# Optimization experiments

Hardware: AMD Instinct MI355X
Metric: run time of the kernel (lower is better)

The kernel has to match this reference:

```python
import jax, jax.numpy as jnp
import numpy as np

LR = 1.0
THRESHOLD = 0.5
EPS = 1e-8


def _hebbian_mask(x, H):
    # x: [B, x_size], H: [y_size, x_size]
    xn = x / jnp.linalg.norm(x, axis=1, keepdims=True)
    y = xn @ H.T                                   # [B, y_size]
    yn = y / jnp.linalg.norm(y, axis=1, keepdims=True)
    theta = jnp.mean(yn ** 2)                      # scalar
    # sum over batch of outer products == GEMM: [y_size, x_size]
    H_new = H + LR * (jnp.einsum('by,bx->yx', yn, xn) - theta * H)
    score = jnp.sum(H_new, axis=1)                 # [y_size]
    score = (score - jnp.min(score)) / (jnp.max(score) - jnp.min(score) + EPS)
    return jnp.where(score < THRESHOLD, 0.0, 1.0).astype(x.dtype)


def setup_inputs() -> dict:
    key = jax.random.key(0)
    ks = jax.random.split(key, 12)
    B, D_IN, D_OUT = 8192, 1024, 1000
    h = [256, 128, 64]
    inp = {
        'x': jax.random.normal(ks[0], (B, D_IN), dtype=jnp.float32),
        'mask0': jnp.ones((h[0],), dtype=jnp.float32),
        'mask1': jnp.ones((h[1],), dtype=jnp.float32),
        'mask2': jnp.ones((h[2],), dtype=jnp.float32),
        # linear layer params (torch Linear: y = x @ W.T + b)
        'W1': jax.random.normal(ks[1], (h[0], D_IN), dtype=jnp.float32) * 0.02,
        'b1': jnp.zeros((h[0],), dtype=jnp.float32),
        'W2': jax.random.normal(ks[2], (h[1], h[0]), dtype=jnp.float32) * 0.02,
        'b2': jnp.zeros((h[1],), dtype=jnp.float32),
        'W3': jax.random.normal(ks[3], (h[2], h[1]), dtype=jnp.float32) * 0.02,
        'b3': jnp.zeros((h[2],), dtype=jnp.float32),
        'W4': jax.random.normal(ks[4], (D_OUT, h[2]), dtype=jnp.float32) * 0.02,
        'b4': jnp.zeros((D_OUT,), dtype=jnp.float32),
        # hebbian params, init N(0, 0.01) as in the module (4th never used in forward)
        'H1': jax.random.normal(ks[5], (h[0], D_IN), dtype=jnp.float32) * 0.01,
        'H2': jax.random.normal(ks[6], (h[1], h[0]), dtype=jnp.float32) * 0.01,
        'H3': jax.random.normal(ks[7], (h[2], h[1]), dtype=jnp.float32) * 0.01,
    }
    return inp


def reference(x, mask0, mask1, mask2, W1, b1, W2, b2, W3, b3, W4, b4, H1, H2, H3):
    # layer 1 (hebbian uses the layer *input*)
    hm0 = _hebbian_mask(x, H1)
    x1 = jax.nn.relu(x @ W1.T + b1) * mask0
    # layer 2
    hm1 = _hebbian_mask(x1, H2)
    x2 = jax.nn.relu(x1 @ W2.T + b2) * mask1
    # layer 3
    hm2 = _hebbian_mask(x2, H3)
    x3 = jax.nn.relu(x2 @ W3.T + b3) * mask2
    # layer 4 (relu applied, no mask, no hebbian)
    out = jax.nn.relu(x3 @ W4.T + b4)
    return (out, hm0, hm1, hm2)
```

## Files before the change

kernel.cpp:

```cpp
#include <hip/hip_runtime.h>
#include <math.h>

typedef __attribute__((ext_vector_type(8))) short short8;
typedef __attribute__((ext_vector_type(4))) float floatx4;

typedef __attribute__((address_space(1))) const unsigned int as1_uint;
typedef __attribute__((address_space(3))) unsigned int as3_uint;
#define GLD16(g, l) __builtin_amdgcn_global_load_lds((as1_uint*)(g), (as3_uint*)(l), 16, 0, 0)

__device__ __forceinline__ unsigned short f2bf(float f) {
    unsigned int u = __float_as_uint(f);
    return (unsigned short)((u + 0x7fffu + ((u >> 16) & 1u)) >> 16);
}
__device__ __forceinline__ float bf2f(unsigned short h) {
    return __uint_as_float(((unsigned int)h) << 16);
}

__global__ __launch_bounds__(256) void convert_x(
    const float* __restrict__ x, unsigned short* __restrict__ Axhl,
    float* __restrict__ rs1, float* __restrict__ rq1,
    float* __restrict__ rs2, float* __restrict__ rq2,
    float* __restrict__ rs3, float* __restrict__ rq3,
    float* __restrict__ score, int* __restrict__ ctr)
{
    const int row = blockIdx.x, tid = threadIdx.x;
    if (row == 0) { score[tid] = 0.f; if (tid < 8) ctr[tid] = 0; }
    if (tid == 0) { rs2[row] = 0.f; rq2[row] = 0.f; rs3[row] = 0.f; rq3[row] = 0.f; }
    float4 v = *(const float4*)(x + (size_t)row * 1024 + (tid << 2));
    ushort4 h, l;
    h.x = f2bf(v.x); l.x = f2bf(v.x - bf2f(h.x));
    h.y = f2bf(v.y); l.y = f2bf(v.y - bf2f(h.y));
    h.z = f2bf(v.z); l.z = f2bf(v.z - bf2f(h.z));
    h.w = f2bf(v.w); l.w = f2bf(v.w - bf2f(h.w));
    *(ushort4*)(Axhl + (size_t)row * 2048 + (tid << 2)) = h;
    *(ushort4*)(Axhl + (size_t)row * 2048 + 1024 + (tid << 2)) = l;
    float s = v.x + v.y + v.z + v.w;
    float qq = v.x*v.x + v.y*v.y + v.z*v.z + v.w*v.w;
#pragma unroll
    for (int d = 1; d < 64; d <<= 1) { s += __shfl_xor(s, d, 64); qq += __shfl_xor(qq, d, 64); }
    __shared__ float sS[4], sQ[4];
    if ((tid & 63) == 0) { sS[tid >> 6] = s; sQ[tid >> 6] = qq; }
    __syncthreads();
    if (tid == 0) {
        rs1[row] = sS[0] + sS[1] + sS[2] + sS[3];
        rq1[row] = sQ[0] + sQ[1] + sQ[2] + sQ[3];
    }
}

__global__ __launch_bounds__(256) void convert_w(
    const float* __restrict__ H1, const float* __restrict__ W1,
    const float* __restrict__ H2, const float* __restrict__ W2,
    const float* __restrict__ H3, const float* __restrict__ W3,
    const float* __restrict__ W4,
    unsigned short* __restrict__ B1, unsigned short* __restrict__ B2,
    unsigned short* __restrict__ B3, unsigned short* __restrict__ B4,
    float* __restrict__ rsH1, float* __restrict__ rsH2, float* __restrict__ rsH3)
{
    const int b = blockIdx.x, tid = threadIdx.x;
    const float* src; unsigned short* dst; int K; float* rsum = nullptr;
    if (b < 256)      { K = 1024; src = H1 + (size_t)b * 1024;        dst = B1 + (size_t)b * 2048;        rsum = rsH1 + b; }
    else if (b < 512) { K = 1024; src = W1 + (size_t)(b - 256) * 1024; dst = B1 + (size_t)b * 2048; }
    else if (b < 640) { K = 256;  src = H2 + (size_t)(b - 512) * 256;  dst = B2 + (size_t)(b - 512) * 512; rsum = rsH2 + (b - 512); }
    else if (b < 768) { K = 256;  src = W2 + (size_t)(b - 640) * 256;  dst = B2 + (size_t)(b - 512) * 512; }
    else if (b < 832) { K = 128;  src = H3 + (size_t)(b - 768) * 128;  dst = B3 + (size_t)(b - 768) * 256; rsum = rsH3 + (b - 768); }
    else if (b < 896) { K = 128;  src = W3 + (size_t)(b - 832) * 128;  dst = B3 + (size_t)(b - 768) * 256; }
    else { K = 64; int r = b - 896; src = (r < 1000) ? (W4 + (size_t)r * 64) : nullptr; dst = B4 + (size_t)r * 128; }

    float lsum = 0.f;
    if (tid * 4 < K) {
        float4 v = src ? *(const float4*)(src + tid * 4) : make_float4(0.f, 0.f, 0.f, 0.f);
        ushort4 h, l;
        h.x = f2bf(v.x); l.x = f2bf(v.x - bf2f(h.x));
        h.y = f2bf(v.y); l.y = f2bf(v.y - bf2f(h.y));
        h.z = f2bf(v.z); l.z = f2bf(v.z - bf2f(h.z));
        h.w = f2bf(v.w); l.w = f2bf(v.w - bf2f(h.w));
        *(ushort4*)(dst + tid * 4) = h;
        *(ushort4*)(dst + K + tid * 4) = l;
        lsum = v.x + v.y + v.z + v.w;
    }
    if (rsum) {
#pragma unroll
        for (int d = 1; d < 64; d <<= 1) lsum += __shfl_xor(lsum, d, 64);
        __shared__ float sS[4];
        if ((tid & 63) == 0) sS[tid >> 6] = lsum;
        __syncthreads();
        if (tid == 0) *rsum = sS[0] + sS[1] + sS[2] + sS[3];
    }
}

template<int TM, int TN>
__global__ __launch_bounds__(256) void mfma_layer(
    const unsigned short* __restrict__ Ag, const unsigned short* __restrict__ Bg,
    const float* __restrict__ bias, const float* __restrict__ maskv,
    float* __restrict__ T, unsigned short* __restrict__ Xhl,
    float* __restrict__ outF,
    float* __restrict__ rs, float* __restrict__ rq,
    int K, int Nh, int Nw, int NwReal)
{
    constexpr int MI = TM / 32;
    constexpr int NJ = TN / 32;
    constexpr int IA = TM / 16;
    constexpr int IB = TN / 16;
    constexpr int NI = 2 * (IA + IB);
    constexpr int PERW = NI / 4;
    constexpr int BUFB = NI * 1024;
    __shared__ __align__(16) char lds[2 * BUFB];

    const int tid = threadIdx.x;
    const int w = tid >> 6, lane = tid & 63;
    const int q = lane >> 4, m16 = lane & 15;
    const int wm = w & 1, wn = w >> 1;

    const int lin = blockIdx.y * gridDim.x + blockIdx.x;
    const int g = lin & 7, idx = lin >> 3;
    const int rows8 = gridDim.y >> 3;
    const int by = g + 8 * (idx % rows8);
    const int bx = idx / rows8;

    const int strideB = 4 * K;
    const int v = lane >> 2, u = lane & 3;

    const char* srcp[PERW];
#pragma unroll
    for (int t0 = 0; t0 < PERW; ++t0) {
        const int t = w * PERW + t0;
        int rloc; const char* base;
        if (t < IA)               { rloc = t * 16 + v;                base = (const char*)Ag + (size_t)(by * TM + rloc) * strideB; }
        else if (t < 2 * IA)      { rloc = (t - IA) * 16 + v;         base = (const char*)Ag + (size_t)(by * TM + rloc) * strideB + 2 * K; }
        else if (t < 2 * IA + IB) { rloc = (t - 2 * IA) * 16 + v;     base = (const char*)Bg + (size_t)(bx * TN + rloc) * strideB; }
        else                      { rloc = (t - 2 * IA - IB) * 16 + v; base = (const char*)Bg + (size_t)(bx * TN + rloc) * strideB + 2 * K; }
        srcp[t0] = base + ((u ^ (rloc & 3)) << 4);
    }

    auto stage = [&](int buf, int k0) {
        char* dst = lds + buf * BUFB + (w * PERW) * 1024;
        const int kb = 2 * k0;
#pragma unroll
        for (int t0 = 0; t0 < PERW; ++t0)
            GLD16(srcp[t0] + kb, dst + t0 * 1024);
    };

    floatx4 acc[MI][NJ] = {};
    const int NIT = K / 32;

    stage(0, 0);
    int cur = 0;
    for (int it = 0; it < NIT; ++it) {
        __syncthreads();
        if (it + 1 < NIT) stage(cur ^ 1, (it + 1) * 32);
        const char* pb = lds + cur * BUFB;
        short8 ah[MI], al[MI], bh[NJ], bl[NJ];
#pragma unroll
        for (int i = 0; i < MI; ++i) {
            const int ra = wm * (TM / 2) + i * 16 + m16;
            const int so = (q ^ (ra & 3)) << 4;
            ah[i] = *(const short8*)(pb + ra * 64 + so);
            al[i] = *(const short8*)(pb + IA * 1024 + ra * 64 + so);
        }
#pragma unroll
        for (int j = 0; j < NJ; ++j) {
            const int rb = wn * (TN / 2) + j * 16 + m16;
            const int so = (q ^ (rb & 3)) << 4;
            bh[j] = *(const short8*)(pb + 2 * IA * 1024 + rb * 64 + so);
            bl[j] = *(const short8*)(pb + (2 * IA + IB) * 1024 + rb * 64 + so);
        }
#pragma unroll
        for (int i = 0; i < MI; ++i)
#pragma unroll
            for (int j = 0; j < NJ; ++j) {
                acc[i][j] = __builtin_amdgcn_mfma_f32_16x16x32_bf16(ah[i], bh[j], acc[i][j], 0, 0, 0);
                acc[i][j] = __builtin_amdgcn_mfma_f32_16x16x32_bf16(al[i], bh[j], acc[i][j], 0, 0, 0);
                acc[i][j] = __builtin_amdgcn_mfma_f32_16x16x32_bf16(ah[i], bl[j], acc[i][j], 0, 0, 0);
            }
        cur ^= 1;
    }

    const int colW = bx * TN + wn * (TN / 2);
    const bool isHwave = (outF == nullptr) && (colW < Nh);
#pragma unroll
    for (int i = 0; i < MI; ++i) {
        const int row0 = by * TM + wm * (TM / 2) + i * 16 + q * 4;
        float rsum[4] = {0.f, 0.f, 0.f, 0.f}, rqsum[4] = {0.f, 0.f, 0.f, 0.f};
#pragma unroll
        for (int j = 0; j < NJ; ++j) {
            const int col = colW + j * 16 + m16;
            floatx4 vv = acc[i][j];
            if (outF) {
                if (col < NwReal) {
                    const float bb = bias[col];
#pragma unroll
                    for (int rg = 0; rg < 4; ++rg)
                        outF[(size_t)(row0 + rg) * NwReal + col] = fmaxf(vv[rg] + bb, 0.f);
                }
            } else if (isHwave) {
#pragma unroll
                for (int rg = 0; rg < 4; ++rg)
                    T[(size_t)(row0 + rg) * Nh + col] = vv[rg];
            } else {
                const int c = col - Nh;
                const float bb = bias[c], mm = maskv[c];
#pragma unroll
                for (int rg = 0; rg < 4; ++rg) {
                    const float xv = fmaxf(vv[rg] + bb, 0.f) * mm;
                    const unsigned short hi = f2bf(xv);
                    const unsigned short lo = f2bf(xv - bf2f(hi));
                    Xhl[(size_t)(row0 + rg) * (2 * Nw) + c] = hi;
                    Xhl[(size_t)(row0 + rg) * (2 * Nw) + Nw + c] = lo;
                    rsum[rg] += xv; rqsum[rg] += xv * xv;
                }
            }
        }
        if (rs && !isHwave && !outF) {
#pragma unroll
            for (int rg = 0; rg < 4; ++rg) {
                float a_ = rsum[rg], b_ = rqsum[rg];
#pragma unroll
                for (int d = 1; d < 16; d <<= 1) {
                    a_ += __shfl_xor(a_, d, 64);
                    b_ += __shfl_xor(b_, d, 64);
                }
                if (m16 == 0) {
                    atomicAdd(&rs[row0 + rg], a_);
                    atomicAdd(&rq[row0 + rg], b_);
                }
            }
        }
    }
}

__global__ __launch_bounds__(256) void hebb_finish(
    const float* __restrict__ T, const float* __restrict__ rs,
    const float* __restrict__ rq, const float* __restrict__ rowsumH,
    float* __restrict__ score, int* __restrict__ counter,
    float* __restrict__ hm, int ysize)
{
    const int tid = threadIdx.x, lane = tid & 63, wave = tid >> 6;
    const int vecsz = ysize >> 6;
    const int b0 = blockIdx.x * 64;
    float accv[4] = {0.f, 0.f, 0.f, 0.f};
    for (int r = wave; r < 64; r += 4) {
        const float* Trow = T + (size_t)(b0 + r) * ysize;
        float vals[4] = {0.f, 0.f, 0.f, 0.f};
        if (vecsz == 4) { float4 t = *(const float4*)(Trow + (lane << 2)); vals[0]=t.x; vals[1]=t.y; vals[2]=t.z; vals[3]=t.w; }
        else if (vecsz == 2) { float2 t = *(const float2*)(Trow + (lane << 1)); vals[0]=t.x; vals[1]=t.y; }
        else vals[0] = Trow[lane];
        float sq = vals[0]*vals[0] + vals[1]*vals[1] + vals[2]*vals[2] + vals[3]*vals[3];
#pragma unroll
        for (int i = 1; i < 64; i <<= 1) sq += __shfl_xor(sq, i, 64);
        const float wgt = rs[b0 + r] / (sqrtf(rq[b0 + r]) * sqrtf(sq));
        for (int j = 0; j < 4; ++j) accv[j] += vals[j] * wgt;
    }
    __shared__ float sPart[4][256];
    for (int j = 0; j < vecsz; ++j) sPart[wave][lane * vecsz + j] = accv[j];
    __syncthreads();
    if (tid < ysize)
        atomicAdd(&score[tid], sPart[0][tid] + sPart[1][tid] + sPart[2][tid] + sPart[3][tid]);
    __syncthreads();
    __shared__ int lastFlag;
    if (tid == 0) {
        __threadfence();
        lastFlag = (atomicAdd(counter, 1) == (int)gridDim.x - 1) ? 1 : 0;
    }
    __syncthreads();
    if (!lastFlag) return;
    float full = 0.f;
    if (tid < ysize) {
        float sc = atomicAdd(&score[tid], 0.f);
        full = (1.f - 1.f / (float)ysize) * rowsumH[tid] + sc;
    }
    __shared__ float sMin[256], sMax[256];
    sMin[tid] = (tid < ysize) ? full : 3.4e38f;
    sMax[tid] = (tid < ysize) ? full : -3.4e38f;
    __syncthreads();
    for (int st = 128; st > 0; st >>= 1) {
        if (tid < st) { sMin[tid] = fminf(sMin[tid], sMin[tid+st]); sMax[tid] = fmaxf(sMax[tid], sMax[tid+st]); }
        __syncthreads();
    }
    if (tid < ysize) {
        float nrm = (full - sMin[0]) / (sMax[0] - sMin[0] + 1e-8f);
        hm[tid] = (nrm < 0.5f) ? 0.f : 1.f;
    }
    score[tid] = 0.f;
}

extern "C" void kernel_launch(void* const* d_in, const int* in_sizes, int n_in,
                              void* d_out, int out_size, void* d_ws, size_t ws_size,
                              hipStream_t stream)
{
    const float* x     = (const float*)d_in[0];
    const float* mask0 = (const float*)d_in[1];
    const float* mask1 = (const float*)d_in[2];
    const float* mask2 = (const float*)d_in[3];
    const float* W1 = (const float*)d_in[4];  const float* b1 = (const float*)d_in[5];
    const float* W2 = (const float*)d_in[6];  const float* b2 = (const float*)d_in[7];
    const float* W3 = (const float*)d_in[8];  const float* b3 = (const float*)d_in[9];
    const float* W4 = (const float*)d_in[10]; const float* b4 = (const float*)d_in[11];
    const float* H1 = (const float*)d_in[12];
    const float* H2 = (const float*)d_in[13];
    const float* H3 = (const float*)d_in[14];

    float* out = (float*)d_out;
    float* hm0 = out + (size_t)8192 * 1000;
    float* hm1 = hm0 + 256;
    float* hm2 = hm1 + 128;

    float* ws = (float*)d_ws;
    unsigned short* Axhl = (unsigned short*)ws;
    unsigned short* X2hl = (unsigned short*)ws;
    unsigned short* X3hl = (unsigned short*)(ws + 1048576);
    float* p = ws + 8388608;
    unsigned short* B1 = (unsigned short*)p;  p += 524288;
    unsigned short* B2 = (unsigned short*)p;  p += 65536;
    unsigned short* B3 = (unsigned short*)p;  p += 16384;
    unsigned short* B4 = (unsigned short*)p;  p += 65536;
    float* T    = p;  p += 2097152;
    unsigned short* X1hl = (unsigned short*)p; p += 2097152;
    float* rs1 = p; p += 8192;  float* rq1 = p; p += 8192;
    float* rs2 = p; p += 8192;  float* rq2 = p; p += 8192;
    float* rs3 = p; p += 8192;  float* rq3 = p; p += 8192;
    float* rsH1 = p; p += 256;  float* rsH2 = p; p += 128;  float* rsH3 = p; p += 64;
    float* score = p; p += 256;
    int* ctr = (int*)p;

    convert_x<<<8192, 256, 0, stream>>>(x, Axhl, rs1, rq1, rs2, rq2, rs3, rq3, score, ctr);
    convert_w<<<1920, 256, 0, stream>>>(H1, W1, H2, W2, H3, W3, W4, B1, B2, B3, B4, rsH1, rsH2, rsH3);

    mfma_layer<128, 64><<<dim3(8, 64), 256, 0, stream>>>(
        Axhl, B1, b1, mask0, T, X1hl, nullptr, rs2, rq2, 1024, 256, 256, 256);
    hebb_finish<<<128, 256, 0, stream>>>(T, rs1, rq1, rsH1, score, ctr + 0, hm0, 256);

    mfma_layer<64, 64><<<dim3(4, 128), 256, 0, stream>>>(
        X1hl, B2, b2, mask1, T, X2hl, nullptr, rs3, rq3, 256, 128, 128, 128);
    hebb_finish<<<128, 256, 0, stream>>>(T, rs2, rq2, rsH2, score, ctr + 1, hm1, 128);

    mfma_layer<64, 64><<<dim3(2, 128), 256, 0, stream>>>(
        X2hl, B3, b3, mask2, T, X3hl, nullptr, nullptr, nullptr, 128, 64, 64, 64);
    hebb_finish<<<128, 256, 0, stream>>>(T, rs3, rq3, rsH3, score, ctr + 2, hm2, 64);

    mfma_layer<128, 64><<<dim3(16, 64), 256, 0, stream>>>(
        X3hl, B4, b4, nullptr, nullptr, nullptr, out, nullptr, nullptr, 64, 0, 1024, 1000);
}
```

Baseline: 225.8 us.

## Merge conversion kernels and fold hebbian reductions into next layer's GEMM launch

Combines the x and weight conversion kernels into one launch. Each hebb_finish reduction now runs as extra leading blocks inside the following layer's GEMM kernel, which needs separate T buffers and score arrays per layer. This cuts the launch count from 9 to 5 and lets the hebbian reduction run alongside the GEMM blocks. The LDS swizzle also changes to XOR with (row>>1)&3, aiming to reduce bank conflicts. The cost is more workspace and hebbian blocks that compete with GEMM blocks for compute units.

```diff
diff --git a/kernel.cpp b/kernel.cpp
--- a/kernel.cpp
+++ b/kernel.cpp
@@ -16,86 +16,147 @@
     return __uint_as_float(((unsigned int)h) << 16);
 }
 
-__global__ __launch_bounds__(256) void convert_x(
+__global__ __launch_bounds__(256) void convert_all(
     const float* __restrict__ x, unsigned short* __restrict__ Axhl,
-    float* __restrict__ rs1, float* __restrict__ rq1,
-    float* __restrict__ rs2, float* __restrict__ rq2,
-    float* __restrict__ rs3, float* __restrict__ rq3,
-    float* __restrict__ score, int* __restrict__ ctr)
-{
-    const int row = blockIdx.x, tid = threadIdx.x;
-    if (row == 0) { score[tid] = 0.f; if (tid < 8) ctr[tid] = 0; }
-    if (tid == 0) { rs2[row] = 0.f; rq2[row] = 0.f; rs3[row] = 0.f; rq3[row] = 0.f; }
-    float4 v = *(const float4*)(x + (size_t)row * 1024 + (tid << 2));
-    ushort4 h, l;
-    h.x = f2bf(v.x); l.x = f2bf(v.x - bf2f(h.x));
-    h.y = f2bf(v.y); l.y = f2bf(v.y - bf2f(h.y));
-    h.z = f2bf(v.z); l.z = f2bf(v.z - bf2f(h.z));
-    h.w = f2bf(v.w); l.w = f2bf(v.w - bf2f(h.w));
-    *(ushort4*)(Axhl + (size_t)row * 2048 + (tid << 2)) = h;
-    *(ushort4*)(Axhl + (size_t)row * 2048 + 1024 + (tid << 2)) = l;
-    float s = v.x + v.y + v.z + v.w;
-    float qq = v.x*v.x + v.y*v.y + v.z*v.z + v.w*v.w;
-#pragma unroll
-    for (int d = 1; d < 64; d <<= 1) { s += __shfl_xor(s, d, 64); qq += __shfl_xor(qq, d, 64); }
-    __shared__ float sS[4], sQ[4];
-    if ((tid & 63) == 0) { sS[tid >> 6] = s; sQ[tid >> 6] = qq; }
-    __syncthreads();
-    if (tid == 0) {
-        rs1[row] = sS[0] + sS[1] + sS[2] + sS[3];
-        rq1[row] = sQ[0] + sQ[1] + sQ[2] + sQ[3];
-    }
-}
-
-__global__ __launch_bounds__(256) void convert_w(
     const float* __restrict__ H1, const float* __restrict__ W1,
     const float* __restrict__ H2, const float* __restrict__ W2,
     const float* __restrict__ H3, const float* __restrict__ W3,
     const float* __restrict__ W4,
     unsigned short* __restrict__ B1, unsigned short* __restrict__ B2,
     unsigned short* __restrict__ B3, unsigned short* __restrict__ B4,
-    float* __restrict__ rsH1, float* __restrict__ rsH2, float* __restrict__ rsH3)
+    float* __restrict__ rs1, float* __restrict__ rq1,
+    float* __restrict__ rs2, float* __restrict__ rq2,
+    float* __restrict__ rs3, float* __restrict__ rq3,
+    float* __restrict__ rsH1, float* __restrict__ rsH2, float* __restrict__ rsH3,
+    float* __restrict__ score1, float* __restrict__ score2,
+    float* __restrict__ score3, int* __restrict__ ctr)
 {
     const int b = blockIdx.x, tid = threadIdx.x;
-    const float* src; unsigned short* dst; int K; float* rsum = nullptr;
-    if (b < 256)      { K = 1024; src = H1 + (size_t)b * 1024;        dst = B1 + (size_t)b * 2048;        rsum = rsH1 + b; }
-    else if (b < 512) { K = 1024; src = W1 + (size_t)(b - 256) * 1024; dst = B1 + (size_t)b * 2048; }
-    else if (b < 640) { K = 256;  src = H2 + (size_t)(b - 512) * 256;  dst = B2 + (size_t)(b - 512) * 512; rsum = rsH2 + (b - 512); }
-    else if (b < 768) { K = 256;  src = W2 + (size_t)(b - 640) * 256;  dst = B2 + (size_t)(b - 512) * 512; }
-    else if (b < 832) { K = 128;  src = H3 + (size_t)(b - 768) * 128;  dst = B3 + (size_t)(b - 768) * 256; rsum = rsH3 + (b - 768); }
-    else if (b < 896) { K = 128;  src = W3 + (size_t)(b - 832) * 128;  dst = B3 + (size_t)(b - 768) * 256; }
-    else { K = 64; int r = b - 896; src = (r < 1000) ? (W4 + (size_t)r * 64) : nullptr; dst = B4 + (size_t)r * 128; }
-
-    float lsum = 0.f;
-    if (tid * 4 < K) {
-        float4 v = src ? *(const float4*)(src + tid * 4) : make_float4(0.f, 0.f, 0.f, 0.f);
+    if (b < 8192) {
+        if (b == 0) {
+            score1[tid] = 0.f; score2[tid] = 0.f; score3[tid] = 0.f;
+            if (tid < 8) ctr[tid] = 0;
+        }
+        if (tid == 0) { rs2[b] = 0.f; rq2[b] = 0.f; rs3[b] = 0.f; rq3[b] = 0.f; }
+        float4 v = *(const float4*)(x + (size_t)b * 1024 + (tid << 2));
         ushort4 h, l;
         h.x = f2bf(v.x); l.x = f2bf(v.x - bf2f(h.x));
         h.y = f2bf(v.y); l.y = f2bf(v.y - bf2f(h.y));
         h.z = f2bf(v.z); l.z = f2bf(v.z - bf2f(h.z));
         h.w = f2bf(v.w); l.w = f2bf(v.w - bf2f(h.w));
-        *(ushort4*)(dst + tid * 4) = h;
-        *(ushort4*)(dst + K + tid * 4) = l;
-        lsum = v.x + v.y + v.z + v.w;
-    }
-    if (rsum) {
-#pragma unroll
-        for (int d = 1; d < 64; d <<= 1) lsum += __shfl_xor(lsum, d, 64);
-        __shared__ float sS[4];
-        if ((tid & 63) == 0) sS[tid >> 6] = lsum;
+        *(ushort4*)(Axhl + (size_t)b * 2048 + (tid << 2)) = h;
+        *(ushort4*)(Axhl + (size_t)b * 2048 + 1024 + (tid << 2)) = l;
+        float s = v.x + v.y + v.z + v.w;
+        float qq = v.x*v.x + v.y*v.y + v.z*v.z + v.w*v.w;
+#pragma unroll
+        for (int d = 1; d < 64; d <<= 1) { s += __shfl_xor(s, d, 64); qq += __shfl_xor(qq, d, 64); }
+        __shared__ float sS[4], sQ[4];
+        if ((tid & 63) == 0) { sS[tid >> 6] = s; sQ[tid >> 6] = qq; }
         __syncthreads();
-        if (tid == 0) *rsum = sS[0] + sS[1] + sS[2] + sS[3];
+        if (tid == 0) {
+            rs1[b] = sS[0] + sS[1] + sS[2] + sS[3];
+            rq1[b] = sQ[0] + sQ[1] + sQ[2] + sQ[3];
+        }
+    } else {
+        const int wb = b - 8192;
+        const float* src; unsigned short* dst; int K; float* rsum = nullptr;
+        if (wb < 256)      { K = 1024; src = H1 + (size_t)wb * 1024;         dst = B1 + (size_t)wb * 2048;        rsum = rsH1 + wb; }
+        else if (wb < 512) { K = 1024; src = W1 + (size_t)(wb - 256) * 1024; dst = B1 + (size_t)wb * 2048; }
+        else if (wb < 640) { K = 256;  src = H2 + (size_t)(wb - 512) * 256;  dst = B2 + (size_t)(wb - 512) * 512; rsum = rsH2 + (wb - 512); }
+        else if (wb < 768) { K = 256;  src = W2 + (size_t)(wb - 640) * 256;  dst = B2 + (size_t)(wb - 512) * 512; }
+        else if (wb < 832) { K = 128;  src = H3 + (size_t)(wb - 768) * 128;  dst = B3 + (size_t)(wb - 768) * 256; rsum = rsH3 + (wb - 768); }
+        else if (wb < 896) { K = 128;  src = W3 + (size_t)(wb - 832) * 128;  dst = B3 + (size_t)(wb - 768) * 256; }
+        else { K = 64; int r = wb - 896; src = (r < 1000) ? (W4 + (size_t)r * 64) : nullptr; dst = B4 + (size_t)r * 128; }
+        float lsum = 0.f;
+        if (tid * 4 < K) {
+            float4 v = src ? *(const float4*)(src + tid * 4) : make_float4(0.f, 0.f, 0.f, 0.f);
+            ushort4 h, l;
+            h.x = f2bf(v.x); l.x = f2bf(v.x - bf2f(h.x));
+            h.y = f2bf(v.y); l.y = f2bf(v.y - bf2f(h.y));
+            h.z = f2bf(v.z); l.z = f2bf(v.z - bf2f(h.z));
+            h.w = f2bf(v.w); l.w = f2bf(v.w - bf2f(h.w));
+            *(ushort4*)(dst + tid * 4) = h;
+            *(ushort4*)(dst + K + tid * 4) = l;
+            lsum = v.x + v.y + v.z + v.w;
+        }
+        if (rsum) {
+#pragma unroll
+            for (int d = 1; d < 64; d <<= 1) lsum += __shfl_xor(lsum, d, 64);
+            __shared__ float sW[4];
+            if ((tid & 63) == 0) sW[tid >> 6] = lsum;
+            __syncthreads();
+            if (tid == 0) *rsum = sW[0] + sW[1] + sW[2] + sW[3];
+        }
+    }
+}
+
+__device__ void hebb_dev(char* smem, int hb,
+    const float* __restrict__ T, const float* __restrict__ rs,
+    const float* __restrict__ rq, const float* __restrict__ rowsumH,
+    float* __restrict__ score, int* __restrict__ counter,
+    float* __restrict__ hm, int ysize, int nHebb)
+{
+    float* sPart = (float*)smem;
+    float* sMin  = sPart + 1024;
+    float* sMax  = sMin + 256;
+    int*   lastFlag = (int*)(sMax + 256);
+    const int tid = threadIdx.x, lane = tid & 63, wave = tid >> 6;
+    const int vecsz = ysize >> 6;
+    const int b0 = hb * 64;
+    float accv[4] = {0.f, 0.f, 0.f, 0.f};
+    for (int r = wave; r < 64; r += 4) {
+        const float* Trow = T + (size_t)(b0 + r) * ysize;
+        float vals[4] = {0.f, 0.f, 0.f, 0.f};
+        if (vecsz == 4)      { float4 t = *(const float4*)(Trow + (lane << 2)); vals[0]=t.x; vals[1]=t.y; vals[2]=t.z; vals[3]=t.w; }
+        else if (vecsz == 2) { float2 t = *(const float2*)(Trow + (lane << 1)); vals[0]=t.x; vals[1]=t.y; }
+        else                 vals[0] = Trow[lane];
+        float sq = vals[0]*vals[0] + vals[1]*vals[1] + vals[2]*vals[2] + vals[3]*vals[3];
+#pragma unroll
+        for (int i = 1; i < 64; i <<= 1) sq += __shfl_xor(sq, i, 64);
+        const float wgt = rs[b0 + r] / (sqrtf(rq[b0 + r]) * sqrtf(sq));
+        for (int j = 0; j < 4; ++j) accv[j] += vals[j] * wgt;
+    }
+    for (int j = 0; j < vecsz; ++j) sPart[wave * 256 + lane * vecsz + j] = accv[j];
+    __syncthreads();
+    if (tid < ysize)
+        atomicAdd(&score[tid], sPart[tid] + sPart[256 + tid] + sPart[512 + tid] + sPart[768 + tid]);
+    __syncthreads();
+    if (tid == 0) {
+        __threadfence();
+        *lastFlag = (atomicAdd(counter, 1) == nHebb - 1) ? 1 : 0;
+    }
+    __syncthreads();
+    if (!*lastFlag) return;
+    float full = 0.f;
+    if (tid < ysize) {
+        float sc = atomicAdd(&score[tid], 0.f);
+        full = (1.f - 1.f / (float)ysize) * rowsumH[tid] + sc;
+    }
+    sMin[tid] = (tid < ysize) ? full : 3.4e38f;
+    sMax[tid] = (tid < ysize) ? full : -3.4e38f;
+    __syncthreads();
+    for (int st = 128; st > 0; st >>= 1) {
+        if (tid < st) { sMin[tid] = fminf(sMin[tid], sMin[tid+st]); sMax[tid] = fmaxf(sMax[tid], sMax[tid+st]); }
+        __syncthreads();
+    }
+    if (tid < ysize) {
+        float nrm = (full - sMin[0]) / (sMax[0] - sMin[0] + 1e-8f);
+        hm[tid] = (nrm < 0.5f) ? 0.f : 1.f;
     }
 }
 
 template<int TM, int TN>
-__global__ __launch_bounds__(256) void mfma_layer(
+__global__ __launch_bounds__(256) void mfma_hebb(
     const unsigned short* __restrict__ Ag, const unsigned short* __restrict__ Bg,
     const float* __restrict__ bias, const float* __restrict__ maskv,
     float* __restrict__ T, unsigned short* __restrict__ Xhl,
     float* __restrict__ outF,
     float* __restrict__ rs, float* __restrict__ rq,
-    int K, int Nh, int Nw, int NwReal)
+    int K, int Nh, int Nw, int NwReal, int ryShift,
+    const float* __restrict__ hT, const float* __restrict__ hrs,
+    const float* __restrict__ hrq, const float* __restrict__ hrsH,
+    float* __restrict__ hscore, int* __restrict__ hctr,
+    float* __restrict__ hhm, int hy, int nHebb)
 {
     constexpr int MI = TM / 32;
     constexpr int NJ = TN / 32;
@@ -106,16 +167,20 @@
     constexpr int BUFB = NI * 1024;
     __shared__ __align__(16) char lds[2 * BUFB];
 
+    if ((int)blockIdx.x < nHebb) {
+        hebb_dev(lds, blockIdx.x, hT, hrs, hrq, hrsH, hscore, hctr, hhm, hy, nHebb);
+        return;
+    }
+
     const int tid = threadIdx.x;
     const int w = tid >> 6, lane = tid & 63;
     const int q = lane >> 4, m16 = lane & 15;
     const int wm = w & 1, wn = w >> 1;
 
-    const int lin = blockIdx.y * gridDim.x + blockIdx.x;
+    const int lin = blockIdx.x - nHebb;
     const int g = lin & 7, idx = lin >> 3;
-    const int rows8 = gridDim.y >> 3;
-    const int by = g + 8 * (idx % rows8);
-    const int bx = idx / rows8;
+    const int by = g + 8 * (idx & ((1 << ryShift) - 1));
+    const int bx = idx >> ryShift;
 
     const int strideB = 4 * K;
     const int v = lane >> 2, u = lane & 3;
@@ -125,11 +190,11 @@
     for (int t0 = 0; t0 < PERW; ++t0) {
         const int t = w * PERW + t0;
         int rloc; const char* base;
-        if (t < IA)               { rloc = t * 16 + v;                base = (const char*)Ag + (size_t)(by * TM + rloc) * strideB; }
-        else if (t < 2 * IA)      { rloc = (t - IA) * 16 + v;         base = (const char*)Ag + (size_t)(by * TM + rloc) * strideB + 2 * K; }
-        else if (t < 2 * IA + IB) { rloc = (t - 2 * IA) * 16 + v;     base = (const char*)Bg + (size_t)(bx * TN + rloc) * strideB; }
+        if (t < IA)               { rloc = t * 16 + v;                 base = (const char*)Ag + (size_t)(by * TM + rloc) * strideB; }
+        else if (t < 2 * IA)      { rloc = (t - IA) * 16 + v;          base = (const char*)Ag + (size_t)(by * TM + rloc) * strideB + 2 * K; }
+        else if (t < 2 * IA + IB) { rloc = (t - 2 * IA) * 16 + v;      base = (const char*)Bg + (size_t)(bx * TN + rloc) * strideB; }
         else                      { rloc = (t - 2 * IA - IB) * 16 + v; base = (const char*)Bg + (size_t)(bx * TN + rloc) * strideB + 2 * K; }
-        srcp[t0] = base + ((u ^ (rloc & 3)) << 4);
+        srcp[t0] = base + ((u ^ ((rloc >> 1) & 3)) << 4);
     }
 
     auto stage = [&](int buf, int k0) {
@@ -153,14 +218,14 @@
 #pragma unroll
         for (int i = 0; i < MI; ++i) {
             const int ra = wm * (TM / 2) + i * 16 + m16;
-            const int so = (q ^ (ra & 3)) << 4;
+            const int so = ((q ^ ((ra >> 1) & 3)) << 4);
             ah[i] = *(const short8*)(pb + ra * 64 + so);
             al[i] = *(const short8*)(pb + IA * 1024 + ra * 64 + so);
         }
 #pragma unroll
         for (int j = 0; j < NJ; ++j) {
             const int rb = wn * (TN / 2) + j * 16 + m16;
-            const int so = (q ^ (rb & 3)) << 4;
+            const int so = ((q ^ ((rb >> 1) & 3)) << 4);
             bh[j] = *(const short8*)(pb + 2 * IA * 1024 + rb * 64 + so);
             bl[j] = *(const short8*)(pb + (2 * IA + IB) * 1024 + rb * 64 + so);
         }
@@ -226,61 +291,6 @@
             }
         }
     }
-}
-
-__global__ __launch_bounds__(256) void hebb_finish(
-    const float* __restrict__ T, const float* __restrict__ rs,
-    const float* __restrict__ rq, const float* __restrict__ rowsumH,
-    float* __restrict__ score, int* __restrict__ counter,
-    float* __restrict__ hm, int ysize)
-{
-    const int tid = threadIdx.x, lane = tid & 63, wave = tid >> 6;
-    const int vecsz = ysize >> 6;
-    const int b0 = blockIdx.x * 64;
-    float accv[4] = {0.f, 0.f, 0.f, 0.f};
-    for (int r = wave; r < 64; r += 4) {
-        const float* Trow = T + (size_t)(b0 + r) * ysize;
-        float vals[4] = {0.f, 0.f, 0.f, 0.f};
-        if (vecsz == 4) { float4 t = *(const float4*)(Trow + (lane << 2)); vals[0]=t.x; vals[1]=t.y; vals[2]=t.z; vals[3]=t.w; }
-        else if (vecsz == 2) { float2 t = *(const float2*)(Trow + (lane << 1)); vals[0]=t.x; vals[1]=t.y; }
-        else vals[0] = Trow[lane];
-        float sq = vals[0]*vals[0] + vals[1]*vals[1] + vals[2]*vals[2] + vals[3]*vals[3];
-#pragma unroll
-        for (int i = 1; i < 64; i <<= 1) sq += __shfl_xor(sq, i, 64);
-        const float wgt = rs[b0 + r] / (sqrtf(rq[b0 + r]) * sqrtf(sq));
-        for (int j = 0; j < 4; ++j) accv[j] += vals[j] * wgt;
-    }
-    __shared__ float sPart[4][256];
-    for (int j = 0; j < vecsz; ++j) sPart[wave][lane * vecsz + j] = accv[j];
-    __syncthreads();
-    if (tid < ysize)
-        atomicAdd(&score[tid], sPart[0][tid] + sPart[1][tid] + sPart[2][tid] + sPart[3][tid]);
-    __syncthreads();
-    __shared__ int lastFlag;
-    if (tid == 0) {
-        __threadfence();
-        lastFlag = (atomicAdd(counter, 1) == (int)gridDim.x - 1) ? 1 : 0;
-    }
-    __syncthreads();
-    if (!lastFlag) return;
-    float full = 0.f;
-    if (tid < ysize) {
-        float sc = atomicAdd(&score[tid], 0.f);
-        full = (1.f - 1.f / (float)ysize) * rowsumH[tid] + sc;
-    }
-    __shared__ float sMin[256], sMax[256];
-    sMin[tid] = (tid < ysize) ? full : 3.4e38f;
-    sMax[tid] = (tid < ysize) ? full : -3.4e38f;
-    __syncthreads();
-    for (int st = 128; st > 0; st >>= 1) {
-        if (tid < st) { sMin[tid] = fminf(sMin[tid], sMin[tid+st]); sMax[tid] = fmaxf(sMax[tid], sMax[tid+st]); }
-        __syncthreads();
-    }
-    if (tid < ysize) {
-        float nrm = (full - sMin[0]) / (sMax[0] - sMin[0] + 1e-8f);
-        hm[tid] = (nrm < 0.5f) ? 0.f : 1.f;
-    }
-    score[tid] = 0.f;
 }
 
 extern "C" void kernel_launch(void* const* d_in, const int* in_sizes, int n_in,
@@ -313,30 +323,41 @@
     unsigned short* B2 = (unsigned short*)p;  p += 65536;
     unsigned short* B3 = (unsigned short*)p;  p += 16384;
     unsigned short* B4 = (unsigned short*)p;  p += 65536;
-    float* T    = p;  p += 2097152;
+    float* T1 = p; p += 2097152;
+    float* T2 = p; p += 1048576;
+    float* T3 = p; p += 524288;
     unsigned short* X1hl = (unsigned short*)p; p += 2097152;
     float* rs1 = p; p += 8192;  float* rq1 = p; p += 8192;
     float* rs2 = p; p += 8192;  float* rq2 = p; p += 8192;
     float* rs3 = p; p += 8192;  float* rq3 = p; p += 8192;
     float* rsH1 = p; p += 256;  float* rsH2 = p; p += 128;  float* rsH3 = p; p += 64;
-    float* score = p; p += 256;
+    float* score1 = p; p += 256;
+    float* score2 = p; p += 256;
+    float* score3 = p; p += 256;
     int* ctr = (int*)p;
 
-    convert_x<<<8192, 256, 0, stream>>>(x, Axhl, rs1, rq1, rs2, rq2, rs3, rq3, score, ctr);
-    convert_w<<<1920, 256, 0, stream>>>(H1, W1, H2, W2, H3, W3, W4, B1, B2, B3, B4, rsH1, rsH2, rsH3);
-
-    mfma_layer<128, 64><<<dim3(8, 64), 256, 0, stream>>>(
-        Axhl, B1, b1, mask0, T, X1hl, nullptr, rs2, rq2, 1024, 256, 256, 256);
-    hebb_finish<<<128, 256, 0, stream>>>(T, rs1, rq1, rsH1, score, ctr + 0, hm0, 256);
-
-    mfma_layer<64, 64><<<dim3(4, 128), 256, 0, stream>>>(
-        X1hl, B2, b2, mask1, T, X2hl, nullptr, rs3, rq3, 256, 128, 128, 128);
-    hebb_finish<<<128, 256, 0, stream>>>(T, rs2, rq2, rsH2, score, ctr + 1, hm1, 128);
-
-    mfma_layer<64, 64><<<dim3(2, 128), 256, 0, stream>>>(
-        X2hl, B3, b3, mask2, T, X3hl, nullptr, nullptr, nullptr, 128, 64, 64, 64);
-    hebb_finish<<<128, 256, 0, stream>>>(T, rs3, rq3, rsH3, score, ctr + 2, hm2, 64);
-
-    mfma_layer<128, 64><<<dim3(16, 64), 256, 0, stream>>>(
-        X3hl, B4, b4, nullptr, nullptr, nullptr, out, nullptr, nullptr, 64, 0, 1024, 1000);
-}
+    convert_all<<<10112, 256, 0, stream>>>(
+        x, Axhl, H1, W1, H2, W2, H3, W3, W4, B1, B2, B3, B4,
+        rs1, rq1, rs2, rq2, rs3, rq3, rsH1, rsH2, rsH3,
+        score1, score2, score3, ctr);
+
+    mfma_hebb<128, 64><<<512, 256, 0, stream>>>(
+        Axhl, B1, b1, mask0, T1, X1hl, nullptr, rs2, rq2,
+        1024, 256, 256, 256, 3,
+        nullptr, nullptr, nullptr, nullptr, nullptr, nullptr, nullptr, 0, 0);
+
+    mfma_hebb<64, 64><<<640, 256, 0, stream>>>(
+        X1hl, B2, b2, mask1, T2, X2hl, nullptr, rs3, rq3,
+        256, 128, 128, 128, 4,
+        T1, rs1, rq1, rsH1, score1, ctr + 0, hm0, 256, 128);
+
+    mfma_hebb<64, 64><<<384, 256, 0, stream>>>(
+        X2hl, B3, b3, mask2, T3, X3hl, nullptr, nullptr, nullptr,
+        128, 64, 64, 64, 4,
+        T2, rs2, rq2, rsH2, score2, ctr + 1, hm1, 128, 128);
+
+    mfma_hebb<128, 64><<<1152, 256, 0, stream>>>(
+        X3hl, B4, b4, nullptr, nullptr, nullptr, out, nullptr, nullptr,
+        64, 0, 1024, 1000, 3,
+        T3, rs3, rq3, rsH3, score3, ctr + 2, hm2, 64, 128);
+}
```

Result: faster. 205.6 us (-8.9%).
